# Kernel tuning notes

Hardware: AMD Instinct MI355X
Metric: run time of the kernel (lower is better)

Reference implementation:

```python
import jax, jax.numpy as jnp
import numpy as np

N_VERTICES = 24  # hardcoded via torch.eye(24) in the original
K = 3


def normalized_adj(adj):
    # scipy version: L = (A @ D^-1/2).T @ D^-1/2 = D^-1/2 @ A^T @ D^-1/2
    d = adj.sum(axis=1)
    d_inv_sqrt = jnp.where(d > 0, 1.0 / jnp.sqrt(d), 0.0)
    return (adj * d_inv_sqrt[None, :]).T * d_inv_sqrt[None, :]


def cheb_polynomials(L, k_order):
    Ts = [jnp.eye(N_VERTICES, dtype=L.dtype), L]
    for _ in range(2, k_order):
        Ts.append(2.0 * L @ Ts[-1] - Ts[-2])
    return jnp.stack(Ts[:k_order])  # (K, N, N)


def setup_inputs() -> dict:
    key = jax.random.key(0)
    k1, k2, k3 = jax.random.split(key, 3)
    x = jax.random.normal(k1, (64, 32, N_VERTICES, 512), dtype=jnp.float32)
    adj = jax.random.uniform(k2, (N_VERTICES, N_VERTICES), dtype=jnp.float32)
    Theta = jax.random.normal(k3, (K, 32, 32), dtype=jnp.float32)
    return {"x": x, "adj": adj, "Theta": Theta}


def reference(x, adj, Theta):
    # x: (b, c, n, t); adj: (n, n); Theta: (K, c, o)
    L = normalized_adj(adj)
    T = cheb_polynomials(L, K)  # (K, n, m)
    # original per-timestep, per-k: rhs[b,m,c] = sum_n x[b,n,c] T_k[n,m];
    # out[b,m,o] += rhs @ Theta_k. Fused over t and k, final permute -> (b,o,m,t).
    out = jnp.einsum('knm,bcnt,kco->bomt', T, x, Theta)
    return out
```

## Files before the change

kernel.cpp:

```cpp
#include <hip/hip_runtime.h>
#include <hip/hip_bf16.h>
#include <stdint.h>


#define NV 24
#define CIN 32
#define COUT 32
#define TDIM 512
#define BATCH 64
#define MDIM 768
#define KD 768
#define BM 128
#define BN 128
#define BK 32
#define NKT (KD / BK)
#define NTT (TDIM / BN)
#define NMT (MDIM / BM)
#define BLOB (BM * BK)
#define BSH (BN * BK)

typedef __attribute__((ext_vector_type(8))) short short8v;
typedef __attribute__((ext_vector_type(4))) float float4v;

union PackU { short8v s; __hip_bfloat162 h[4]; };

__device__ inline unsigned short f2bf(float f) {
    unsigned int u = __float_as_uint(f);
    unsigned int r = (u + 0x7fffu + ((u >> 16) & 1u)) >> 16;
    return (unsigned short)r;
}

__global__ __launch_bounds__(256) void prep_w(const float* __restrict__ adj,
                                              const float* __restrict__ Theta,
                                              unsigned short* __restrict__ Wp) {
    __shared__ float adjS[NV * NV];
    __shared__ float disS[NV];
    __shared__ float LS[NV * NV];
    __shared__ float T2S[NV * NV];
    int tid = threadIdx.x;
    for (int e = tid; e < NV * NV; e += 256) adjS[e] = adj[e];
    __syncthreads();
    if (tid < NV) {
        float d = 0.f;
        for (int j = 0; j < NV; ++j) d += adjS[tid * NV + j];
        disS[tid] = (d > 0.f) ? rsqrtf(d) : 0.f;
    }
    __syncthreads();
    for (int e = tid; e < NV * NV; e += 256) {
        int i = e / NV, j = e % NV;
        LS[e] = disS[i] * adjS[j * NV + i] * disS[j];
    }
    __syncthreads();
    for (int e = tid; e < NV * NV; e += 256) {
        int i = e / NV, j = e % NV;
        float s = 0.f;
        for (int p = 0; p < NV; ++p) s += LS[i * NV + p] * LS[p * NV + j];
        T2S[e] = 2.f * s - (i == j ? 1.f : 0.f);
    }
    __syncthreads();
    int r0 = blockIdx.x * (MDIM / 64);
    for (int e = tid; e < (MDIM / 64) * KD; e += 256) {
        int lr = e / KD, col = e % KD;
        int row = r0 + lr;
        int o = row / NV, m = row % NV;
        int c = col / NV, n = col % NV;
        float th0 = Theta[0 * CIN * COUT + c * COUT + o];
        float th1 = Theta[1 * CIN * COUT + c * COUT + o];
        float th2 = Theta[2 * CIN * COUT + c * COUT + o];
        float v = (n == m ? th0 : 0.f) + LS[n * NV + m] * th1 + T2S[n * NV + m] * th2;
        size_t idx = (((size_t)(row >> 7) * NKT + (col >> 5)) * BM + (row & 127)) * BK + (col & 31);
        Wp[idx] = f2bf(v);
    }
}

#define STEP(KT, BUF, XC, AC, AN)                                              \
    do {                                                                       \
        PackU u0, u1;                                                          \
        _Pragma("unroll")                                                      \
        for (int i = 0; i < 4; ++i) {                                          \
            u0.h[i] = __float22bfloat162_rn({XC[2 * i], XC[2 * i + 1]});       \
            u1.h[i] = __float22bfloat162_rn({XC[8 + 2 * i], XC[8 + 2 * i + 1]}); \
        }                                                                      \
        *(short8v*)(Bs + (BUF) * BSH + wr0) = u0.s;                            \
        *(short8v*)(Bs + (BUF) * BSH + wr0 + 64 * BK) = u1.s;                  \
        if ((KT) + 1 < NKT) {          \
            const short8v* Ap_ = (const short8v*)(Ab + (size_t)((KT) + 1) * BLOB); \
            _Pragma("unroll")                                                  \
            for (int i = 0; i < 4; ++i) AN[i] = Ap_[afr + i * 64];             \
        }                                                                      \
        if ((KT) + 2 < NKT) {  \
            const float* xr_ = xb + (size_t)(((KT) + 2) * BK + kq * 8) * TDIM; \
            _Pragma("unroll")                                                  \
            for (int kk = 0; kk < 8; ++kk) {                                   \
                XC[kk] = xr_[(size_t)kk * TDIM + tp];                          \
                XC[8 + kk] = xr_[(size_t)kk * TDIM + tp + 64];                 \
            }                                                                  \
        }                                                                      \
        __syncthreads();  \
        short8v bb[4];                                                         \
        _Pragma("unroll")                                                      \
        for (int j = 0; j < 4; ++j)                                            \
            bb[j] = *(const short8v*)(Bs + (BUF) * BSH + rb + j * (16 * BK));  \
        _Pragma("unroll")                                                      \
        for (int i = 0; i < 4; ++i)                                            \
            _Pragma("unroll")                                                  \
            for (int j = 0; j < 4; ++j)                                        \
                acc[i][j] = __builtin_amdgcn_mfma_f32_16x16x32_bf16(           \
                    AC[i], bb[j], acc[i][j], 0, 0, 0);                         \
    } while (0)

__global__ __launch_bounds__(256, 3) void gemm_fused(const unsigned short* __restrict__ Wp,
                                                     const float* __restrict__ x,
                                                     float* __restrict__ out) {
    __shared__ __attribute__((aligned(16))) unsigned short Bs[2 * BSH];

    int id = blockIdx.x;
    int hi = id / 48;
    int rem = id - hi * 48;
    int mt = rem >> 3;
    int g = hi * 8 + (rem & 7);
    int b = g >> 2;
    int tt = g & 3;

    int tid = threadIdx.x;
    int wave = tid >> 6;
    int lane = tid & 63;
    int quad = lane >> 4;
    int l16 = lane & 15;
    int wm = wave >> 1, wn = wave & 1;
    int kq = wave;
    int tp = lane;

    const unsigned short* Ab = Wp + (size_t)mt * NKT * BLOB;
    const float* xb = x + (size_t)b * KD * TDIM + tt * BN;

    int wr0 = (tp * BK + kq * 8) ^ ((tp & 7) * 8);
    int rb = ((wn * 64 + l16) * BK + quad * 8) ^ ((l16 & 7) * 8);
    int afr = (wm * 64 + l16) * 4 + quad;

    const float4v zero4 = {0.f, 0.f, 0.f, 0.f};
    float4v acc[4][4];
#pragma unroll
    for (int i = 0; i < 4; ++i)
#pragma unroll
        for (int j = 0; j < 4; ++j) acc[i][j] = zero4;

    float XrA[16], XrB[16];
    short8v Aev[4], Aod[4];

    {
        const float* xr = xb + (size_t)(kq * 8) * TDIM;
#pragma unroll
        for (int kk = 0; kk < 8; ++kk) {
            XrA[kk] = xr[(size_t)kk * TDIM + tp];
            XrA[8 + kk] = xr[(size_t)kk * TDIM + tp + 64];
        }
        const short8v* Ap = (const short8v*)Ab;
#pragma unroll
        for (int i = 0; i < 4; ++i) Aev[i] = Ap[afr + i * 64];
        const float* xr1 = xb + (size_t)(BK + kq * 8) * TDIM;
#pragma unroll
        for (int kk = 0; kk < 8; ++kk) {
            XrB[kk] = xr1[(size_t)kk * TDIM + tp];
            XrB[8 + kk] = xr1[(size_t)kk * TDIM + tp + 64];
        }
    }

    for (int kt = 0; kt < NKT; kt += 2) {
        STEP(kt, 0, XrA, Aev, Aod);
        STEP(kt + 1, 1, XrB, Aod, Aev);
    }

    float* outB = out + (size_t)b * MDIM * TDIM;
    int rbase = mt * BM + wm * 64;
    int cbase = tt * BN + wn * 64;
#pragma unroll
    for (int i = 0; i < 4; ++i) {
#pragma unroll
        for (int j = 0; j < 4; ++j) {
            int row0 = rbase + i * 16 + quad * 4;
            int col = cbase + j * 16 + l16;
#pragma unroll
            for (int r = 0; r < 4; ++r)
                __builtin_nontemporal_store(acc[i][j][r],
                                            &outB[(size_t)(row0 + r) * TDIM + col]);
        }
    }
}

extern "C" void kernel_launch(void* const* d_in, const int* in_sizes, int n_in,
                              void* d_out, int out_size, void* d_ws, size_t ws_size,
                              hipStream_t stream) {
    const float* x = (const float*)d_in[0];
    const float* adj = (const float*)d_in[1];
    const float* Theta = (const float*)d_in[2];
    float* out = (float*)d_out;

    unsigned short* Wp = (unsigned short*)d_ws;

    prep_w<<<64, 256, 0, stream>>>(adj, Theta, Wp);
    gemm_fused<<<NMT * NTT * BATCH, 256, 0, stream>>>(Wp, x, out);
}
```

Before: 233.7 us.

## Compute full M per block with whole-K x slab staged in LDS

Each block now owns one batch and a 64-column time slice and computes all 768 output rows with 8 waves. It first stages the entire K=768 x slab into LDS as bf16, using a float staging buffer for a coalesced transpose. After that the main loop streams only the weight tiles, so each x element is read from global memory once instead of once per M tile. The cost is a large LDS footprint, an un-overlapped load prologue, and more accumulator registers per wave.

After: 234.8 us. No clear change (+0.5%).

```diff
diff --git a/kernel.cpp b/kernel.cpp
--- a/kernel.cpp
+++ b/kernel.cpp
@@ -10,19 +10,16 @@
 #define BATCH 64
 #define MDIM 768
 #define KD 768
-#define BM 128
-#define BN 128
 #define BK 32
 #define NKT (KD / BK)
-#define NTT (TDIM / BN)
-#define NMT (MDIM / BM)
+#define BM 128
 #define BLOB (BM * BK)
-#define BSH (BN * BK)
+#define BT 64
+#define KUN (KD / 8)
+#define FSTR 66
 
 typedef __attribute__((ext_vector_type(8))) short short8v;
 typedef __attribute__((ext_vector_type(4))) float float4v;
-
-union PackU { short8v s; __hip_bfloat162 h[4]; };
 
 __device__ inline unsigned short f2bf(float f) {
     unsigned int u = __float_as_uint(f);
@@ -73,113 +70,109 @@
     }
 }
 
-#define STEP(KT, BUF, XC, AC, AN)                                              \
+#define GSTEP(KT, AC, AN)                                                      \
     do {                                                                       \
-        PackU u0, u1;                                                          \
-        _Pragma("unroll")                                                      \
-        for (int i = 0; i < 4; ++i) {                                          \
-            u0.h[i] = __float22bfloat162_rn({XC[2 * i], XC[2 * i + 1]});       \
-            u1.h[i] = __float22bfloat162_rn({XC[8 + 2 * i], XC[8 + 2 * i + 1]}); \
-        }                                                                      \
-        *(short8v*)(Bs + (BUF) * BSH + wr0) = u0.s;                            \
-        *(short8v*)(Bs + (BUF) * BSH + wr0 + 64 * BK) = u1.s;                  \
-        if ((KT) + 1 < NKT) {          \
-            const short8v* Ap_ = (const short8v*)(Ab + (size_t)((KT) + 1) * BLOB); \
-            _Pragma("unroll")                                                  \
-            for (int i = 0; i < 4; ++i) AN[i] = Ap_[afr + i * 64];             \
-        }                                                                      \
-        if ((KT) + 2 < NKT) {  \
-            const float* xr_ = xb + (size_t)(((KT) + 2) * BK + kq * 8) * TDIM; \
-            _Pragma("unroll")                                                  \
-            for (int kk = 0; kk < 8; ++kk) {                                   \
-                XC[kk] = xr_[(size_t)kk * TDIM + tp];                          \
-                XC[8 + kk] = xr_[(size_t)kk * TDIM + tp + 64];                 \
-            }                                                                  \
-        }                                                                      \
-        __syncthreads();  \
+        int kx = (((KT) * 4 + quad) ^ s7);                                     \
         short8v bb[4];                                                         \
         _Pragma("unroll")                                                      \
-        for (int j = 0; j < 4; ++j)                                            \
-            bb[j] = *(const short8v*)(Bs + (BUF) * BSH + rb + j * (16 * BK));  \
+        for (int j = 0; j < 4; ++j) bb[j] = Bsv[tj[j] + kx];                   \
+        if ((KT) + 1 < NKT) {                                                  \
+            _Pragma("unroll")                                                  \
+            for (int i = 0; i < 6; ++i) AN[i] = Apv[aoff[i] + ((KT) + 1) * 512]; \
+        }                                                                      \
         _Pragma("unroll")                                                      \
-        for (int i = 0; i < 4; ++i)                                            \
+        for (int i = 0; i < 6; ++i)                                            \
             _Pragma("unroll")                                                  \
             for (int j = 0; j < 4; ++j)                                        \
                 acc[i][j] = __builtin_amdgcn_mfma_f32_16x16x32_bf16(           \
                     AC[i], bb[j], acc[i][j], 0, 0, 0);                         \
     } while (0)
 
-__global__ __launch_bounds__(256, 3) void gemm_fused(const unsigned short* __restrict__ Wp,
+__global__ __launch_bounds__(512, 2) void gemm_fullm(const unsigned short* __restrict__ Wp,
                                                      const float* __restrict__ x,
                                                      float* __restrict__ out) {
-    __shared__ __attribute__((aligned(16))) unsigned short Bs[2 * BSH];
+    __shared__ __attribute__((aligned(16))) unsigned short Bs[BT * KUN * 8];
+    __shared__ float LSf[192 * FSTR];
 
     int id = blockIdx.x;
-    int hi = id / 48;
-    int rem = id - hi * 48;
-    int mt = rem >> 3;
-    int g = hi * 8 + (rem & 7);
-    int b = g >> 2;
-    int tt = g & 3;
-
+    int b = id >> 3;
+    int tt = id & 7;
     int tid = threadIdx.x;
-    int wave = tid >> 6;
+    int w = tid >> 6;
     int lane = tid & 63;
     int quad = lane >> 4;
     int l16 = lane & 15;
-    int wm = wave >> 1, wn = wave & 1;
-    int kq = wave;
-    int tp = lane;
+    int t = lane;
+    int s7 = l16 & 7;
 
-    const unsigned short* Ab = Wp + (size_t)mt * NKT * BLOB;
-    const float* xb = x + (size_t)b * KD * TDIM + tt * BN;
+    const float* xg = x + (size_t)b * KD * TDIM + (size_t)tt * BT;
+    short8v* Bsv = (short8v*)Bs;
 
-    int wr0 = (tp * BK + kq * 8) ^ ((tp & 7) * 8);
-    int rb = ((wn * 64 + l16) * BK + quad * 8) ^ ((l16 & 7) * 8);
-    int afr = (wm * 64 + l16) * 4 + quad;
+    for (int kc = 0; kc < 4; ++kc) {
+        float2 v[12];
+#pragma unroll
+        for (int p = 0; p < 12; ++p) {
+            int idx = p * 512 + tid;
+            int kloc = idx >> 5, c2 = idx & 31;
+            v[p] = *(const float2*)(xg + (size_t)(kc * 192 + kloc) * TDIM + c2 * 2);
+        }
+#pragma unroll
+        for (int p = 0; p < 12; ++p) {
+            int idx = p * 512 + tid;
+            int kloc = idx >> 5, c2 = idx & 31;
+            *(float2*)(&LSf[kloc * FSTR + c2 * 2]) = v[p];
+        }
+        __syncthreads();
+#pragma unroll
+        for (int c = 0; c < 3; ++c) {
+            union { short8v s; __hip_bfloat162 h[4]; } u;
+#pragma unroll
+            for (int p = 0; p < 4; ++p) {
+                float f0 = LSf[(w * 24 + c * 8 + 2 * p) * FSTR + t];
+                float f1 = LSf[(w * 24 + c * 8 + 2 * p + 1) * FSTR + t];
+                u.h[p] = __float22bfloat162_rn({f0, f1});
+            }
+            int ku = kc * 24 + w * 3 + c;
+            Bsv[t * KUN + (ku ^ (t & 7))] = u.s;
+        }
+        __syncthreads();
+    }
+
+    const short8v* Apv = (const short8v*)Wp;
+    int aoff[6];
+#pragma unroll
+    for (int i = 0; i < 6; ++i) {
+        int r = w * 96 + i * 16 + l16;
+        aoff[i] = (r >> 7) * (NKT * 512) + (r & 127) * 4 + quad;
+    }
+    int tj[4];
+#pragma unroll
+    for (int j = 0; j < 4; ++j) tj[j] = (j * 16 + l16) * KUN;
 
     const float4v zero4 = {0.f, 0.f, 0.f, 0.f};
-    float4v acc[4][4];
+    float4v acc[6][4];
 #pragma unroll
-    for (int i = 0; i < 4; ++i)
+    for (int i = 0; i < 6; ++i)
 #pragma unroll
         for (int j = 0; j < 4; ++j) acc[i][j] = zero4;
 
-    float XrA[16], XrB[16];
-    short8v Aev[4], Aod[4];
+    short8v Aev[6], Aod[6];
+#pragma unroll
+    for (int i = 0; i < 6; ++i) Aev[i] = Apv[aoff[i]];
 
-    {
-        const float* xr = xb + (size_t)(kq * 8) * TDIM;
-#pragma unroll
-        for (int kk = 0; kk < 8; ++kk) {
-            XrA[kk] = xr[(size_t)kk * TDIM + tp];
-            XrA[8 + kk] = xr[(size_t)kk * TDIM + tp + 64];
-        }
-        const short8v* Ap = (const short8v*)Ab;
-#pragma unroll
-        for (int i = 0; i < 4; ++i) Aev[i] = Ap[afr + i * 64];
-        const float* xr1 = xb + (size_t)(BK + kq * 8) * TDIM;
-#pragma unroll
-        for (int kk = 0; kk < 8; ++kk) {
-            XrB[kk] = xr1[(size_t)kk * TDIM + tp];
-            XrB[8 + kk] = xr1[(size_t)kk * TDIM + tp + 64];
-        }
+    for (int kt = 0; kt < NKT; kt += 2) {
+        GSTEP(kt, Aev, Aod);
+        GSTEP(kt + 1, Aod, Aev);
     }
 
-    for (int kt = 0; kt < NKT; kt += 2) {
-        STEP(kt, 0, XrA, Aev, Aod);
-        STEP(kt + 1, 1, XrB, Aod, Aev);
-    }
-
-    float* outB = out + (size_t)b * MDIM * TDIM;
-    int rbase = mt * BM + wm * 64;
-    int cbase = tt * BN + wn * 64;
+    float* outB = out + (size_t)b * MDIM * TDIM + (size_t)tt * BT;
+    int rb0 = w * 96;
 #pragma unroll
-    for (int i = 0; i < 4; ++i) {
+    for (int i = 0; i < 6; ++i) {
 #pragma unroll
         for (int j = 0; j < 4; ++j) {
-            int row0 = rbase + i * 16 + quad * 4;
-            int col = cbase + j * 16 + l16;
+            int row0 = rb0 + i * 16 + quad * 4;
+            int col = j * 16 + l16;
 #pragma unroll
             for (int r = 0; r < 4; ++r)
                 __builtin_nontemporal_store(acc[i][j][r],
@@ -199,5 +192,5 @@
     unsigned short* Wp = (unsigned short*)d_ws;
 
     prep_w<<<64, 256, 0, stream>>>(adj, Theta, Wp);
-    gemm_fused<<<NMT * NTT * BATCH, 256, 0, stream>>>(Wp, x, out);
+    gemm_fullm<<<BATCH * (TDIM / BT), 512, 0, stream>>>(Wp, x, out);
 }
```
